# Kernel tuning notes

Hardware: AMD Instinct MI355X
Metric: run time of the kernel (lower is better)

The kernel has to match this reference:

```python
import jax, jax.numpy as jnp
import numpy as np

B, S, D, H = 4, 1024, 1024, 16
HD = D // H
EPS = 1e-5


def layer_norm(x, scale, shift):
    mean = jnp.mean(x, axis=-1, keepdims=True)
    var = jnp.mean((x - mean) ** 2, axis=-1, keepdims=True)
    return scale * (x - mean) / jnp.sqrt(var + EPS) + shift


def gelu_tanh(x):
    c = jnp.sqrt(jnp.asarray(2.0 / jnp.pi, dtype=x.dtype))
    return 0.5 * x * (1.0 + jnp.tanh(c * (x + 0.044715 * x ** 3)))


def setup_inputs() -> dict:
    key = jax.random.key(0)
    ks = jax.random.split(key, 12)
    s = 0.02
    return {
        "x": jax.random.normal(ks[0], (B, S, D), dtype=jnp.float32),
        "attention_mask": jnp.ones((B, S), dtype=jnp.int32),
        "wq": jax.random.normal(ks[1], (D, D), dtype=jnp.float32) * s,
        "wk": jax.random.normal(ks[2], (D, D), dtype=jnp.float32) * s,
        "wv": jax.random.normal(ks[3], (D, D), dtype=jnp.float32) * s,
        "wo": jax.random.normal(ks[4], (D, D), dtype=jnp.float32) * s,
        "bo": jnp.zeros((D,), dtype=jnp.float32),
        "ln1_scale": jnp.ones((D,), dtype=jnp.float32),
        "ln1_shift": jnp.zeros((D,), dtype=jnp.float32),
        "ln2_scale": jnp.ones((D,), dtype=jnp.float32),
        "ln2_shift": jnp.zeros((D,), dtype=jnp.float32),
        "w1": jax.random.normal(ks[5], (D, 4 * D), dtype=jnp.float32) * s,
        "b1": jnp.zeros((4 * D,), dtype=jnp.float32),
        "w2": jax.random.normal(ks[6], (4 * D, D), dtype=jnp.float32) * s,
        "b2": jnp.zeros((D,), dtype=jnp.float32),
    }


def reference(x, attention_mask, wq, wk, wv, wo, bo, ln1_scale, ln1_shift,
              ln2_scale, ln2_shift, w1, b1, w2, b2):
    b, s, d = x.shape
    # --- pre-norm attention ---
    shortcut = x
    h = layer_norm(x, ln1_scale, ln1_shift)
    q = (h @ wq).reshape(b, s, H, HD).transpose(0, 2, 1, 3)  # bhsd
    k = (h @ wk).reshape(b, s, H, HD).transpose(0, 2, 1, 3)
    v = (h @ wv).reshape(b, s, H, HD).transpose(0, 2, 1, 3)
    scores = jnp.einsum('bhqd,bhkd->bhqk', q, k)
    causal = jnp.triu(jnp.ones((s, s), dtype=bool), k=1)  # True above diag -> masked
    neg_inf = jnp.asarray(-jnp.inf, dtype=scores.dtype)
    scores = jnp.where(causal, neg_inf, scores)
    pad = attention_mask[:, None, None, :].astype(bool)  # (b,1,1,k)
    scores = jnp.where(pad, scores, neg_inf)
    attn = jax.nn.softmax(scores / jnp.sqrt(jnp.asarray(HD, dtype=scores.dtype)), axis=-1)
    ctx = jnp.einsum('bhqk,bhkd->bhqd', attn, v)
    ctx = ctx.transpose(0, 2, 1, 3).reshape(b, s, d)
    x = shortcut + (ctx @ wo + bo)
    # --- pre-norm FFN ---
    shortcut = x
    h = layer_norm(x, ln2_scale, ln2_shift)
    h = gelu_tanh(h @ w1 + b1) @ w2 + b2
    return shortcut + h
```

## Files before the change

kernel.cpp:

```cpp
#include <hip/hip_runtime.h>
#include <hip/hip_bf16.h>
#include <math.h>

#define B_ 4
#define S_ 1024
#define D_ 1024
#define H_ 16
#define HD_ 64

typedef __hip_bfloat16 bf16_t;
typedef __attribute__((ext_vector_type(8))) short bf16x8;
typedef __attribute__((ext_vector_type(4))) float floatx4;

__device__ __forceinline__ float bf2f(ushort u) {
  return __uint_as_float((unsigned)u << 16);
}

__global__ __launch_bounds__(256) void prep_kernel(
    const float* __restrict__ x, const float* __restrict__ ln1s,
    const float* __restrict__ ln1b, bf16_t* __restrict__ h,
    const float* __restrict__ wq, const float* __restrict__ wk,
    const float* __restrict__ wv, const float* __restrict__ wo,
    const float* __restrict__ w1, const float* __restrict__ w2,
    bf16_t* __restrict__ wqkv_t, bf16_t* __restrict__ wo_t,
    bf16_t* __restrict__ w1_t, bf16_t* __restrict__ w2_t) {
  const int id = blockIdx.x;
  if (id < 4096) {
    const int row = id;
    float4 v = ((const float4*)(x + (size_t)row * D_))[threadIdx.x];
    float s = v.x + v.y + v.z + v.w;
    float ss = v.x * v.x + v.y * v.y + v.z * v.z + v.w * v.w;
#pragma unroll
    for (int off = 32; off > 0; off >>= 1) {
      s += __shfl_xor(s, off);
      ss += __shfl_xor(ss, off);
    }
    __shared__ float ls[4], lss[4], stats[2];
    const int wave = threadIdx.x >> 6, lane = threadIdx.x & 63;
    if (lane == 0) { ls[wave] = s; lss[wave] = ss; }
    __syncthreads();
    if (threadIdx.x == 0) {
      float t = ls[0] + ls[1] + ls[2] + ls[3];
      float tt = lss[0] + lss[1] + lss[2] + lss[3];
      float mean = t * (1.0f / D_);
      stats[0] = mean;
      stats[1] = rsqrtf(tt * (1.0f / D_) - mean * mean + 1e-5f);
    }
    __syncthreads();
    const float mean = stats[0], rstd = stats[1];
    float4 sc = ((const float4*)ln1s)[threadIdx.x];
    float4 sh = ((const float4*)ln1b)[threadIdx.x];
    bf16_t ob[4];
    ob[0] = __float2bfloat16(sc.x * (v.x - mean) * rstd + sh.x);
    ob[1] = __float2bfloat16(sc.y * (v.y - mean) * rstd + sh.y);
    ob[2] = __float2bfloat16(sc.z * (v.z - mean) * rstd + sh.z);
    ob[3] = __float2bfloat16(sc.w * (v.w - mean) * rstd + sh.w);
    *(ushort4*)(h + (size_t)row * D_ + threadIdx.x * 4) = *(ushort4*)ob;
    return;
  }
  const float* W;
  bf16_t* Wt;
  int K, N, n0, k0;
  if (id < 8192) {
    const int t = id - 4096, which = t >> 10, tile = t & 1023;
    n0 = (tile & 31) * 32;
    k0 = (tile >> 5) * 32;
    K = 1024; N = 1024;
    W = which == 0 ? wq : which == 1 ? wk : which == 2 ? wv : wo;
    Wt = which < 3 ? wqkv_t + (size_t)which * 1024 * 1024 : wo_t;
  } else if (id < 12288) {
    const int tile = id - 8192;
    n0 = (tile & 127) * 32;
    k0 = (tile >> 7) * 32;
    K = 1024; N = 4096;
    W = w1; Wt = w1_t;
  } else {
    const int tile = id - 12288;
    n0 = (tile & 31) * 32;
    k0 = (tile >> 5) * 32;
    K = 4096; N = 1024;
    W = w2; Wt = w2_t;
  }
  __shared__ float t[32][33];
  const int lx = threadIdx.x & 31, ly = threadIdx.x >> 5;
#pragma unroll
  for (int r = ly; r < 32; r += 8) t[r][lx] = W[(size_t)(k0 + r) * N + n0 + lx];
  __syncthreads();
#pragma unroll
  for (int r = ly; r < 32; r += 8)
    Wt[(size_t)(n0 + r) * K + k0 + lx] = __float2bfloat16(t[lx][r]);
}

__global__ __launch_bounds__(256) void mgemm_kernel(const bf16_t* __restrict__ A,
                                                    const bf16_t* __restrict__ Bt,
                                                    const float* __restrict__ bias,
                                                    void* __restrict__ C,
                                                    int M, int N, int K, int Kc,
                                                    int Mt, int Nt, int PM,
                                                    int mode) {
  __shared__ bf16_t As[128 * 64];
  __shared__ bf16_t Bs[128 * 64];
  const int tid = threadIdx.x;
  const int lane = tid & 63, w = tid >> 6;

  const int flat = blockIdx.x;
  const int xcd = flat & 7;
  int t0 = flat >> 3;
  const int mb = xcd % PM, nb = xcd / PM;
  const int mt = mb * Mt + (t0 % Mt);
  t0 /= Mt;
  const int nt = nb * Nt + (t0 % Nt);
  const int z = t0 / Nt;
  const int m0 = mt * 128, n0 = nt * 128;
  const int kz0 = z * Kc;
  const int wm = (w >> 1) * 64, wn = (w & 1) * 64;

  floatx4 zero = {0.f, 0.f, 0.f, 0.f};
  floatx4 acc[4][4];
#pragma unroll
  for (int i = 0; i < 4; i++)
#pragma unroll
    for (int j = 0; j < 4; j++) acc[i][j] = zero;

  const int ro8 = lane >> 3;
  const int g8 = ((lane & 7) ^ ro8) * 8;
  const bf16_t* ga[4];
  const bf16_t* gb[4];
  bf16_t* la[4];
  bf16_t* lb[4];
#pragma unroll
  for (int t = 0; t < 4; t++) {
    const int c = w + 4 * t;
    ga[t] = A + (size_t)(m0 + c * 8 + ro8) * K + g8;
    gb[t] = Bt + (size_t)(n0 + c * 8 + ro8) * K + g8;
    la[t] = &As[c * 512];
    lb[t] = &Bs[c * 512];
  }

  const int fr = lane & 15, quad = lane >> 4;

  for (int k0 = kz0; k0 < kz0 + Kc; k0 += 64) {
    __syncthreads();
#pragma unroll
    for (int t = 0; t < 4; t++) {
      __builtin_amdgcn_global_load_lds(
          (const __attribute__((address_space(1))) void*)(ga[t] + k0),
          (__attribute__((address_space(3))) void*)la[t], 16, 0, 0);
      __builtin_amdgcn_global_load_lds(
          (const __attribute__((address_space(1))) void*)(gb[t] + k0),
          (__attribute__((address_space(3))) void*)lb[t], 16, 0, 0);
    }
    __syncthreads();

#pragma unroll
    for (int ks = 0; ks < 2; ks++) {
      const int sq = ((quad + 4 * ks) ^ (fr & 7)) * 8;
      bf16x8 af[4], bfr[4];
#pragma unroll
      for (int i = 0; i < 4; i++) {
        af[i] = *(const bf16x8*)&As[(wm + i * 16 + fr) * 64 + sq];
        bfr[i] = *(const bf16x8*)&Bs[(wn + i * 16 + fr) * 64 + sq];
      }
#pragma unroll
      for (int i = 0; i < 4; i++)
#pragma unroll
        for (int j = 0; j < 4; j++)
          acc[i][j] = __builtin_amdgcn_mfma_f32_16x16x32_bf16(af[i], bfr[j],
                                                              acc[i][j], 0, 0, 0);
    }
  }

  bf16_t* Pz = (mode == 4) ? ((bf16_t*)C + (size_t)z * M * N) : nullptr;
#pragma unroll
  for (int j = 0; j < 4; j++) {
    const int col = n0 + wn + j * 16 + fr;
    const float bj = bias ? bias[col] : 0.f;
#pragma unroll
    for (int i = 0; i < 4; i++) {
      const int rbase = m0 + wm + i * 16 + quad * 4;
#pragma unroll
      for (int r = 0; r < 4; r++) {
        const int row = rbase + r;
        float c = acc[i][j][r] + bj;
        if (mode == 1) {
          const float xg = c;
          const float t = 0.7978845608028654f * (xg + 0.044715f * xg * xg * xg);
          const float th = 2.0f / (1.0f + __expf(-2.0f * t)) - 1.0f;
          c = 0.5f * xg * (1.0f + th);
        }
        if (mode == 4) {
          Pz[(size_t)row * N + col] = __float2bfloat16(c);
        } else {
          ((bf16_t*)C)[(size_t)row * N + col] = __float2bfloat16(c);
        }
      }
    }
  }
}

__global__ __launch_bounds__(256) void reduce2_ln_kernel(
    const bf16_t* __restrict__ P, size_t slice, const float* __restrict__ x,
    const float* __restrict__ bias, const float* __restrict__ scale,
    const float* __restrict__ shift, float* __restrict__ out,
    bf16_t* __restrict__ h) {
  const int row = blockIdx.x;
  const size_t e = (size_t)row * D_ + threadIdx.x * 4;
  const float4 xv = *(const float4*)(x + e);
  const ushort4 p0 = *(const ushort4*)((const ushort*)P + e);
  const ushort4 p1 = *(const ushort4*)((const ushort*)P + slice + e);
  const float4 bb = *(const float4*)(bias + threadIdx.x * 4);
  float4 v;
  v.x = xv.x + bf2f(p0.x) + bf2f(p1.x) + bb.x;
  v.y = xv.y + bf2f(p0.y) + bf2f(p1.y) + bb.y;
  v.z = xv.z + bf2f(p0.z) + bf2f(p1.z) + bb.z;
  v.w = xv.w + bf2f(p0.w) + bf2f(p1.w) + bb.w;
  *(float4*)(out + e) = v;

  float s = v.x + v.y + v.z + v.w;
  float ss = v.x * v.x + v.y * v.y + v.z * v.z + v.w * v.w;
#pragma unroll
  for (int off = 32; off > 0; off >>= 1) {
    s += __shfl_xor(s, off);
    ss += __shfl_xor(ss, off);
  }
  __shared__ float ls[4], lss[4], stats[2];
  const int wave = threadIdx.x >> 6, lane = threadIdx.x & 63;
  if (lane == 0) { ls[wave] = s; lss[wave] = ss; }
  __syncthreads();
  if (threadIdx.x == 0) {
    float t = ls[0] + ls[1] + ls[2] + ls[3];
    float tt = lss[0] + lss[1] + lss[2] + lss[3];
    float mean = t * (1.0f / D_);
    stats[0] = mean;
    stats[1] = rsqrtf(tt * (1.0f / D_) - mean * mean + 1e-5f);
  }
  __syncthreads();
  const float mean = stats[0], rstd = stats[1];
  const float4 sc = *(const float4*)(scale + threadIdx.x * 4);
  const float4 sh = *(const float4*)(shift + threadIdx.x * 4);
  bf16_t ob[4];
  ob[0] = __float2bfloat16(sc.x * (v.x - mean) * rstd + sh.x);
  ob[1] = __float2bfloat16(sc.y * (v.y - mean) * rstd + sh.y);
  ob[2] = __float2bfloat16(sc.z * (v.z - mean) * rstd + sh.z);
  ob[3] = __float2bfloat16(sc.w * (v.w - mean) * rstd + sh.w);
  *(ushort4*)(h + e) = *(ushort4*)ob;
}

__global__ __launch_bounds__(256) void reduce4_kernel(const bf16_t* __restrict__ P,
                                                      size_t slice,
                                                      const float* __restrict__ bias,
                                                      float* __restrict__ out,
                                                      int N) {
  const size_t e = ((size_t)blockIdx.x * 256 + threadIdx.x) * 4;
  const ushort* Pu = (const ushort*)P;
  const ushort4 p0 = *(const ushort4*)(Pu + e);
  const ushort4 p1 = *(const ushort4*)(Pu + slice + e);
  const ushort4 p2 = *(const ushort4*)(Pu + 2 * slice + e);
  const ushort4 p3 = *(const ushort4*)(Pu + 3 * slice + e);
  const float4 r = *(const float4*)(out + e);
  const float4 bb = *(const float4*)(bias + (int)(e % N));
  float4 o;
  o.x = r.x + bb.x + bf2f(p0.x) + bf2f(p1.x) + bf2f(p2.x) + bf2f(p3.x);
  o.y = r.y + bb.y + bf2f(p0.y) + bf2f(p1.y) + bf2f(p2.y) + bf2f(p3.y);
  o.z = r.z + bb.z + bf2f(p0.z) + bf2f(p1.z) + bf2f(p2.z) + bf2f(p3.z);
  o.w = r.w + bb.w + bf2f(p0.w) + bf2f(p1.w) + bf2f(p2.w) + bf2f(p3.w);
  *(float4*)(out + e) = o;
}

__global__ __launch_bounds__(256) void fattn_kernel(const bf16_t* __restrict__ QK,
                                                    const bf16_t* __restrict__ VT,
                                                    const int* __restrict__ mask,
                                                    bf16_t* __restrict__ O) {
  const int qt = gridDim.x - 1 - blockIdx.x;
  const int h = blockIdx.y, b = blockIdx.z;
  const int tid = threadIdx.x;
  const int lane = tid & 63, w = tid >> 6;
  const int tx = lane & 15, quad = lane >> 4;
  const int q0 = qt * 64;

  __shared__ bf16_t Ks[64 * 64];
  __shared__ bf16_t Vs[64 * 64];
  __shared__ ushort Ps[64 * 64];

  const int ro8 = lane >> 3;
  const int g8 = ((lane & 7) ^ ro8) * 8;
  const bf16_t* gk[2];
  const bf16_t* gv[2];
  bf16_t* lk[2];
  bf16_t* lv[2];
#pragma unroll
  for (int t = 0; t < 2; t++) {
    const int c = w + 4 * t;
    gk[t] = QK + (size_t)((size_t)b * S_ + c * 8 + ro8) * 2048 + 1024 + h * HD_ + g8;
    gv[t] = VT + (size_t)(h * HD_ + c * 8 + ro8) * 4096 + (size_t)b * S_ + g8;
    lk[t] = &Ks[c * 512];
    lv[t] = &Vs[c * 512];
  }

  bf16x8 qf[2];
#pragma unroll
  for (int ks = 0; ks < 2; ks++)
    qf[ks] = *(const bf16x8*)(QK + (size_t)((size_t)b * S_ + q0 + w * 16 + tx) * 2048 +
                              h * HD_ + ks * 32 + quad * 8);

  const short oneb = 0x3F80;
  bf16x8 vones = {oneb, oneb, oneb, oneb, oneb, oneb, oneb, oneb};

  floatx4 ctx[4], lacc;
#pragma unroll
  for (int nt = 0; nt < 4; nt++) {
    ctx[nt].x = 0.f; ctx[nt].y = 0.f; ctx[nt].z = 0.f; ctx[nt].w = 0.f;
  }
  lacc.x = 0.f; lacc.y = 0.f; lacc.z = 0.f; lacc.w = 0.f;

  for (int kt = 0; kt <= qt; kt++) {
    const int k0 = kt * 64;
    __syncthreads();
#pragma unroll
    for (int t = 0; t < 2; t++) {
      __builtin_amdgcn_global_load_lds(
          (const __attribute__((address_space(1))) void*)(gk[t] + (size_t)k0 * 2048),
          (__attribute__((address_space(3))) void*)lk[t], 16, 0, 0);
      __builtin_amdgcn_global_load_lds(
          (const __attribute__((address_space(1))) void*)(gv[t] + k0),
          (__attribute__((address_space(3))) void*)lv[t], 16, 0, 0);
    }
    __syncthreads();

    floatx4 accS[4];
#pragma unroll
    for (int nt = 0; nt < 4; nt++) {
      accS[nt].x = 0.f; accS[nt].y = 0.f; accS[nt].z = 0.f; accS[nt].w = 0.f;
    }
#pragma unroll
    for (int ks = 0; ks < 2; ks++) {
      const int sq = ((quad + 4 * ks) ^ (tx & 7)) * 8;
      bf16x8 kf[4];
#pragma unroll
      for (int nt = 0; nt < 4; nt++)
        kf[nt] = *(const bf16x8*)&Ks[(nt * 16 + tx) * 64 + sq];
#pragma unroll
      for (int nt = 0; nt < 4; nt++)
        accS[nt] = __builtin_amdgcn_mfma_f32_16x16x32_bf16(qf[ks], kf[nt],
                                                           accS[nt], 0, 0, 0);
    }

#pragma unroll
    for (int nt = 0; nt < 4; nt++) {
      const int jc = k0 + nt * 16 + tx;
      const bool ok = mask[b * S_ + jc] != 0;
      const int col = nt * 16 + tx;
#pragma unroll
      for (int r = 0; r < 4; r++) {
        const int qq = quad * 4 + r;
        const int qrow = q0 + w * 16 + qq;
        float p = exp2f(accS[nt][r] * 0.1803368801111244f);
        if (jc > qrow || !ok) p = 0.f;
        const int pc = ((((col >> 3) ^ (qq & 7)) << 3)) | (col & 7);
        Ps[(w * 16 + qq) * 64 + pc] =
            ((__hip_bfloat16_raw)__float2bfloat16(p)).x;
      }
    }

#pragma unroll
    for (int ks = 0; ks < 2; ks++) {
      const int sq = ((quad + 4 * ks) ^ (tx & 7)) * 8;
      const bf16x8 pf = *(const bf16x8*)&Ps[(w * 16 + tx) * 64 + sq];
      bf16x8 vf[4];
#pragma unroll
      for (int nt = 0; nt < 4; nt++)
        vf[nt] = *(const bf16x8*)&Vs[(nt * 16 + tx) * 64 + sq];
#pragma unroll
      for (int nt = 0; nt < 4; nt++)
        ctx[nt] = __builtin_amdgcn_mfma_f32_16x16x32_bf16(pf, vf[nt],
                                                          ctx[nt], 0, 0, 0);
      lacc = __builtin_amdgcn_mfma_f32_16x16x32_bf16(pf, vones, lacc, 0, 0, 0);
    }
  }

  const size_t obase = (size_t)b * S_ * D_ + (size_t)h * HD_;
  float rinv[4];
#pragma unroll
  for (int r = 0; r < 4; r++) rinv[r] = 1.0f / lacc[r];
#pragma unroll
  for (int nt = 0; nt < 4; nt++)
#pragma unroll
    for (int r = 0; r < 4; r++) {
      const int q = q0 + w * 16 + quad * 4 + r;
      O[obase + (size_t)q * D_ + nt * 16 + tx] =
          __float2bfloat16(ctx[nt][r] * rinv[r]);
    }
}

extern "C" void kernel_launch(void* const* d_in, const int* in_sizes, int n_in,
                              void* d_out, int out_size, void* d_ws, size_t ws_size,
                              hipStream_t stream) {
  const float* x = (const float*)d_in[0];
  const int* mask = (const int*)d_in[1];
  const float* wq = (const float*)d_in[2];
  const float* wk = (const float*)d_in[3];
  const float* wv = (const float*)d_in[4];
  const float* wo = (const float*)d_in[5];
  const float* bo = (const float*)d_in[6];
  const float* ln2s = (const float*)d_in[9];
  const float* ln2b = (const float*)d_in[10];
  const float* w1 = (const float*)d_in[11];
  const float* b1 = (const float*)d_in[12];
  const float* w2 = (const float*)d_in[13];
  const float* b2 = (const float*)d_in[14];
  float* out = (float*)d_out;

  const int M = B_ * S_;
  char* ws = (char*)d_ws;
  const size_t MB = (size_t)1 << 20;
  bf16_t* qk = (bf16_t*)(ws);
  bf16_t* vT = (bf16_t*)(ws + 16 * MB);
  bf16_t* ffn1 = (bf16_t*)(ws);
  bf16_t* ctx = (bf16_t*)(ws + 32 * MB);
  bf16_t* h = (bf16_t*)(ws + 40 * MB);
  bf16_t* wqkv_t = (bf16_t*)(ws + 48 * MB);
  bf16_t* wo_t = (bf16_t*)(ws + 54 * MB);
  bf16_t* w1_t = (bf16_t*)(ws + 56 * MB);
  bf16_t* w2_t = (bf16_t*)(ws + 64 * MB);
  bf16_t* Pa = (bf16_t*)(ws);
  bf16_t* Pf = (bf16_t*)(ws + 32 * MB);
  const size_t slice = (size_t)M * D_;

  prep_kernel<<<dim3(16384), 256, 0, stream>>>(x, (const float*)d_in[7],
                                               (const float*)d_in[8], h, wq, wk,
                                               wv, wo, w1, w2, wqkv_t, wo_t,
                                               w1_t, w2_t);

  mgemm_kernel<<<dim3(16 * 32), 256, 0, stream>>>(
      h, wqkv_t, nullptr, qk, M, 2 * D_, D_, D_, 8, 8, 4, 0);

  mgemm_kernel<<<dim3(8 * 32), 256, 0, stream>>>(
      wqkv_t + (size_t)2 * 1024 * 1024, h, nullptr, vT, D_, M, D_, D_,
      4, 8, 2, 0);

  fattn_kernel<<<dim3(S_ / 64, H_, B_), 256, 0, stream>>>(qk, vT, mask, ctx);

  mgemm_kernel<<<dim3(8 * 32 * 2), 256, 0, stream>>>(
      ctx, wo_t, nullptr, Pa, M, D_, D_, D_ / 2, 4, 8, 8, 4);

  reduce2_ln_kernel<<<dim3(M), 256, 0, stream>>>(Pa, slice, x, bo, ln2s, ln2b,
                                                 out, h);

  mgemm_kernel<<<dim3(32 * 32), 256, 0, stream>>>(
      h, w1_t, b1, ffn1, M, 4 * D_, D_, D_, 16, 8, 2, 1);

  mgemm_kernel<<<dim3(8 * 32 * 4), 256, 0, stream>>>(
      ffn1, w2_t, nullptr, Pf, M, D_, 4 * D_, D_, 8, 4, 4, 4);

  reduce4_kernel<<<dim3((size_t)M * D_ / 1024), 256, 0, stream>>>(
      Pf, slice, b2, out, D_);
}
```

Baseline: 362.4 us.

## Add 256x256-tile GEMM kernel with 512 threads for FFN matmuls

Introduces a new GEMM kernel using 256x256 output tiles, 8 waves per block, double-buffered direct global-to-LDS loads with XOR swizzle, and uses it for both FFN projections. The larger tiles raise arithmetic intensity and cut global/L2 traffic per MFMA compared with the previous smaller-tile kernel. The FFN1 and split-K FFN2 launches drop to 256 blocks each, which risks lower occupancy, more register pressure (128 accumulator floats per lane), and roughly one wave of blocks across the CUs.

```diff
diff --git a/kernel.cpp b/kernel.cpp
--- a/kernel.cpp
+++ b/kernel.cpp
@@ -198,6 +198,122 @@
   }
 }
 
+__global__ __launch_bounds__(512, 2) void mgemm256_kernel(
+    const bf16_t* __restrict__ A, const bf16_t* __restrict__ Bt,
+    const float* __restrict__ bias, void* __restrict__ C, int M, int N, int K,
+    int Kc, int Mt, int Nt, int PM, int mode) {
+  __shared__ bf16_t sm[2][2][256 * 64];
+  const int tid = threadIdx.x;
+  const int lane = tid & 63, w = tid >> 6;
+
+  const int flat = blockIdx.x;
+  const int xcd = flat & 7;
+  int t0 = flat >> 3;
+  const int mb = xcd % PM, nb = xcd / PM;
+  const int mt = mb * Mt + (t0 % Mt);
+  t0 /= Mt;
+  const int nt = nb * Nt + (t0 % Nt);
+  const int z = t0 / Nt;
+  const int m0 = mt * 256, n0 = nt * 256;
+  const int kz0 = z * Kc;
+  const int wr = w >> 2, wc = w & 3;
+
+  floatx4 zero = {0.f, 0.f, 0.f, 0.f};
+  floatx4 acc[8][4];
+#pragma unroll
+  for (int i = 0; i < 8; i++)
+#pragma unroll
+    for (int j = 0; j < 4; j++) acc[i][j] = zero;
+
+  const int ro8 = lane >> 3;
+  const int g8 = ((lane & 7) ^ ro8) * 8;
+  const bf16_t* gAb = A + (size_t)(m0 + w * 8 + ro8) * K + g8;
+  const bf16_t* gBb = Bt + (size_t)(n0 + w * 8 + ro8) * K + g8;
+  const size_t cstride = (size_t)64 * K;
+
+  auto STAGE = [&](int bufi, int kk) {
+#pragma unroll
+    for (int tt = 0; tt < 4; ++tt) {
+      __builtin_amdgcn_global_load_lds(
+          (const __attribute__((address_space(1))) void*)(gAb + kk +
+                                                          (size_t)tt * cstride),
+          (__attribute__((address_space(3))) void*)&sm[bufi][0][w * 512 +
+                                                                tt * 4096],
+          16, 0, 0);
+      __builtin_amdgcn_global_load_lds(
+          (const __attribute__((address_space(1))) void*)(gBb + kk +
+                                                          (size_t)tt * cstride),
+          (__attribute__((address_space(3))) void*)&sm[bufi][1][w * 512 +
+                                                                tt * 4096],
+          16, 0, 0);
+    }
+  };
+
+  const int fr = lane & 15, quad = lane >> 4;
+  const int ntk = Kc >> 6;
+
+  STAGE(0, kz0);
+  if (ntk > 1) STAGE(1, kz0 + 64);
+
+  for (int t = 0; t < ntk; ++t) {
+    if (t + 1 < ntk) {
+      asm volatile("s_waitcnt vmcnt(8)" ::: "memory");
+    } else {
+      asm volatile("s_waitcnt vmcnt(0)" ::: "memory");
+    }
+    __builtin_amdgcn_s_barrier();
+    const int bi = t & 1;
+#pragma unroll
+    for (int ks = 0; ks < 2; ks++) {
+      const int sq = ((quad + 4 * ks) ^ (fr & 7)) * 8;
+      bf16x8 bfr[4];
+#pragma unroll
+      for (int j = 0; j < 4; j++)
+        bfr[j] = *(const bf16x8*)&sm[bi][1][(wc * 64 + j * 16 + fr) * 64 + sq];
+#pragma unroll
+      for (int mi = 0; mi < 2; mi++) {
+        bf16x8 af[4];
+#pragma unroll
+        for (int i = 0; i < 4; i++)
+          af[i] = *(const bf16x8*)&sm[bi][0]
+                      [(wr * 128 + mi * 64 + i * 16 + fr) * 64 + sq];
+#pragma unroll
+        for (int i = 0; i < 4; i++)
+#pragma unroll
+          for (int j = 0; j < 4; j++)
+            acc[mi * 4 + i][j] = __builtin_amdgcn_mfma_f32_16x16x32_bf16(
+                af[i], bfr[j], acc[mi * 4 + i][j], 0, 0, 0);
+      }
+    }
+    asm volatile("s_waitcnt lgkmcnt(0)" ::: "memory");
+    __builtin_amdgcn_sched_barrier(0);
+    __builtin_amdgcn_s_barrier();
+    if (t + 2 < ntk) STAGE(bi, kz0 + (t + 2) * 64);
+  }
+
+  bf16_t* Pz = (mode == 4) ? ((bf16_t*)C + (size_t)z * M * N) : (bf16_t*)C;
+#pragma unroll
+  for (int j = 0; j < 4; j++) {
+    const int col = n0 + wc * 64 + j * 16 + fr;
+    const float bj = bias ? bias[col] : 0.f;
+#pragma unroll
+    for (int i = 0; i < 8; i++) {
+      const int rbase = m0 + wr * 128 + i * 16 + quad * 4;
+#pragma unroll
+      for (int r = 0; r < 4; r++) {
+        float c = acc[i][j][r] + bj;
+        if (mode == 1) {
+          const float xg = c;
+          const float t2 = 0.7978845608028654f * (xg + 0.044715f * xg * xg * xg);
+          const float th = 2.0f / (1.0f + __expf(-2.0f * t2)) - 1.0f;
+          c = 0.5f * xg * (1.0f + th);
+        }
+        Pz[(size_t)(rbase + r) * N + col] = __float2bfloat16(c);
+      }
+    }
+  }
+}
+
 __global__ __launch_bounds__(256) void reduce2_ln_kernel(
     const bf16_t* __restrict__ P, size_t slice, const float* __restrict__ x,
     const float* __restrict__ bias, const float* __restrict__ scale,
@@ -446,11 +562,11 @@
   reduce2_ln_kernel<<<dim3(M), 256, 0, stream>>>(Pa, slice, x, bo, ln2s, ln2b,
                                                  out, h);
 
-  mgemm_kernel<<<dim3(32 * 32), 256, 0, stream>>>(
-      h, w1_t, b1, ffn1, M, 4 * D_, D_, D_, 16, 8, 2, 1);
-
-  mgemm_kernel<<<dim3(8 * 32 * 4), 256, 0, stream>>>(
-      ffn1, w2_t, nullptr, Pf, M, D_, 4 * D_, D_, 8, 4, 4, 4);
+  mgemm256_kernel<<<dim3(256), 512, 0, stream>>>(
+      h, w1_t, b1, ffn1, M, 4 * D_, D_, D_, 4, 8, 4, 1);
+
+  mgemm256_kernel<<<dim3(256), 512, 0, stream>>>(
+      ffn1, w2_t, nullptr, Pf, M, D_, 4 * D_, D_, 2, 4, 8, 4);
 
   reduce4_kernel<<<dim3((size_t)M * D_ / 1024), 256, 0, stream>>>(
       Pf, slice, b2, out, D_);
```

Measured after the change: 348.8 us. 1.04x faster.
